# Kernel optimization log

Measured on AMD Instinct MI355X. Metric: run time of the kernel, lower is better.

Reference implementation:

```python
import jax, jax.numpy as jnp
import numpy as np

NUM_BINS = 8
TAIL = 3.0
MBW = 1e-3  # min_bin_width
MBH = 1e-3  # min_bin_height
MD = 1e-3   # min_derivative
B, C, H, W = 16, 12, 128, 128
COND = C // 3
HID = 64
STEP = 3 * NUM_BINS - 1
OUT = C * STEP


def setup_inputs() -> dict:
    key = jax.random.key(0)
    ks = jax.random.split(key, 8)
    s = lambda k, shape, scale=1.0: jax.random.normal(k, shape, jnp.float32) * scale
    return {
        'x': s(ks[0], (B, C, H, W)),
        'logdet': jnp.zeros((B,), jnp.float32),
        'conditioning': s(ks[1], (B, COND, H, W)),
        'W1': s(ks[2], (HID, C + COND, 3, 3), 0.05), 'b1': jnp.zeros((HID,), jnp.float32),
        'W2': s(ks[3], (HID, HID, 1, 1), 0.05), 'b2': jnp.zeros((HID,), jnp.float32),
        'W3': s(ks[4], (OUT, HID, 3, 3), 0.05), 'b3': jnp.zeros((OUT,), jnp.float32),
    }


def _conv(x, w, b, pad):
    y = jax.lax.conv_general_dilated(x, w, (1, 1), [(pad, pad), (pad, pad)],
                                     dimension_numbers=('NCHW', 'OIHW', 'NCHW'))
    return y + b[None, :, None, None]


def _checker_mask(h, w, parity):
    ii, jj = jnp.meshgrid(jnp.arange(h), jnp.arange(w), indexing='ij')
    m = jnp.where((ii + jj) % 2 == 0, parity, 1 - parity)
    return m.astype(jnp.float32)[None, None]  # (1,1,H,W)


def _rqs_forward(x, uw, uh, ud):
    # x: (B,C,H,W); uw/uh: (...,K); ud: (...,K-1). 'linear' tails, tail_bound=TAIL.
    K = NUM_BINS
    left, right = -TAIL, TAIL
    inside = (x >= left) & (x <= right)
    xc = jnp.clip(x, left, right)

    w = MBW + (1.0 - MBW * K) * jax.nn.softmax(uw, axis=-1)
    cw = jnp.pad(jnp.cumsum(w, -1), [(0, 0)] * (w.ndim - 1) + [(1, 0)])
    cw = (right - left) * cw + left
    cw = cw.at[..., 0].set(left).at[..., -1].set(right)
    w = cw[..., 1:] - cw[..., :-1]

    h = MBH + (1.0 - MBH * K) * jax.nn.softmax(uh, axis=-1)
    ch = jnp.pad(jnp.cumsum(h, -1), [(0, 0)] * (h.ndim - 1) + [(1, 0)])
    ch = (right - left) * ch + left
    ch = ch.at[..., 0].set(left).at[..., -1].set(right)
    h = ch[..., 1:] - ch[..., :-1]

    const = float(np.log(np.expm1(1.0 - MD)))  # boundary derivative -> 1 under linear tails
    udp = jnp.pad(ud, [(0, 0)] * (ud.ndim - 1) + [(1, 1)], constant_values=const)
    d = MD + jax.nn.softplus(udp)  # (...,K+1)

    delta = h / w
    # searchsorted: bin index per element
    idx = jnp.clip(jnp.sum((xc[..., None] >= cw).astype(jnp.int32), -1) - 1, 0, K - 1)[..., None]
    g = lambda t: jnp.take_along_axis(t, idx, axis=-1)[..., 0]

    icw, iw = g(cw), g(w)
    ich, ih = g(ch), g(h)
    idl = g(delta)
    id0 = g(d)
    id1 = g(d[..., 1:])

    theta = (xc - icw) / iw
    t1 = theta * (1.0 - theta)
    num = ih * (idl * theta ** 2 + id0 * t1)
    den = idl + (id0 + id1 - 2.0 * idl) * t1
    y = ich + num / den
    dnum = idl ** 2 * (id1 * theta ** 2 + 2.0 * idl * t1 + id0 * (1.0 - theta) ** 2)
    lad = jnp.log(dnum) - 2.0 * jnp.log(den)
    return jnp.where(inside, y, x), jnp.where(inside, lad, 0.0)


def reference(x, logdet, conditioning, W1, b1, W2, b2, W3, b3):
    mask = _checker_mask(H, W, 0)
    x_frozen = mask * x
    x_active = (1.0 - mask) * x
    z = jnp.concatenate([x_frozen, conditioning], axis=1)
    h1 = jax.nn.relu(_conv(z, W1, b1, 1))
    h2 = jax.nn.relu(_conv(h1, W2, b2, 0))
    params = _conv(h2, W3, b3, 1)  # (B, C*STEP, H, W)
    # all channels at once instead of python loop over C
    p = params.reshape(B, C, STEP, H, W).transpose(0, 1, 3, 4, 2)  # (B,C,H,W,STEP)
    uw = p[..., :NUM_BINS]
    uh = p[..., NUM_BINS:2 * NUM_BINS]
    ud = p[..., 2 * NUM_BINS:]
    y, lad = _rqs_forward(x_active, uw, uh, ud)
    x_out = x_frozen + y  # matches original: frozen part + spline output (no re-masking of y)
    logdet_out = logdet + lad.sum(axis=(1, 2, 3))
    return x_out, logdet_out
```

## Files before the change

kernel.cpp:

```cpp
#include <hip/hip_runtime.h>

#define HW (128*128)

typedef __bf16 bf16x8 __attribute__((ext_vector_type(8)));
typedef float  float4v __attribute__((ext_vector_type(4)));
typedef int    int4v   __attribute__((ext_vector_type(4)));
typedef int    int2v   __attribute__((ext_vector_type(2)));

static __device__ __forceinline__ short f2bf(float f) {
    unsigned u = __float_as_uint(f);
    unsigned r = (u + 0x7FFFu + ((u >> 16) & 1u)) >> 16;
    return (short)(r & 0xFFFFu);
}
static __device__ __forceinline__ int pack2(short a, short b) {
    return (int)((unsigned short)a | ((unsigned)(unsigned short)b << 16));
}
static __device__ __forceinline__ void async_cp16(const void* g, void* l) {
    __builtin_amdgcn_global_load_lds(
        (const __attribute__((address_space(1))) unsigned int*)g,
        (__attribute__((address_space(3))) unsigned int*)l, 16, 0, 0);
}

__global__ __launch_bounds__(256) void prep_weights(
    const float* __restrict__ W1, const float* __restrict__ W2,
    const float* __restrict__ W3,
    short* __restrict__ W1sw, short* __restrict__ W2sw, short* __restrict__ W3sw,
    char* __restrict__ h2p, int4v* __restrict__ zerobuf)
{
    int tid = blockIdx.x * 256 + threadIdx.x;
    int stride = gridDim.x * 256;
    for (int i = tid; i < 5*256*8; i += stride) {
        int e = i & 7, q = (i >> 3) & 255, s = i >> 11;
        int n = q >> 2, c = q & 3;
        int gc = c ^ ((n >> 1) & 3);
        int tap = 2*s + (gc >> 1);
        int ch = (gc & 1)*8 + e;
        float v = 0.f;
        if (tap < 9) {
            int ky = (tap*11) >> 5; int kx = tap - 3*ky;
            v = W1[((n*16 + ch)*3 + ky)*3 + kx];
        }
        W1sw[i] = f2bf(v);
    }
    for (int i = tid; i < 2*256*8; i += stride) {
        int e = i & 7, q = (i >> 3) & 255, s = i >> 11;
        int n = q >> 2, c = q & 3;
        int gc = c ^ ((n >> 1) & 3);
        int k = s*32 + gc*8 + e;
        W2sw[i] = f2bf(W2[n*64 + k]);
    }
    for (int i = tid; i < 9*288*64; i += stride) {
        int e = i & 7;
        int c = (i >> 3) & 7;
        int r = i >> 6;
        int tap = r / 288;
        int n = r - tap*288;
        int ch = n / 24, jj = n - 24*ch;
        int ci = ((c ^ (n & 7)) << 3) + e;
        float v = 0.f;
        if (jj < 23) v = W3[((ch*23 + jj)*64 + ci)*9 + tap];
        W3sw[i] = f2bf(v);
    }
    for (int i = tid; i < 64; i += stride) { int4v zz = {0,0,0,0}; zerobuf[i] = zz; }
    for (int i = tid; i < 16*516*8; i += stride) {
        int cchunk = i & 7, pxi = (i >> 3) % 516, b = i / (516*8);
        int yy, xx;
        if (pxi < 130)      { yy = 0;   xx = pxi; }
        else if (pxi < 260) { yy = 129; xx = pxi - 130; }
        else if (pxi < 388) { yy = pxi - 260 + 1; xx = 0; }
        else                { yy = pxi - 388 + 1; xx = 129; }
        int4v zz = {0,0,0,0};
        *(int4v*)(h2p + (size_t)((b*130 + yy)*130 + xx)*128 + cchunk*16) = zz;
    }
}

__global__ __launch_bounds__(256) void pack_z(
    const float* __restrict__ x, const float* __restrict__ cond,
    short* __restrict__ zp, float* __restrict__ ldslots)
{
    int id = blockIdx.x * 256 + threadIdx.x;
    if (id < 1024) ldslots[id] = 0.f;
    if (id >= 16*130*130) return;
    int b = id / 16900;
    int rem = id - b*16900;
    int yy = rem / 130;
    int xx = rem - yy*130;
    short vs[16];
    #pragma unroll
    for (int c = 0; c < 16; ++c) vs[c] = 0;
    if (yy >= 1 && yy <= 128 && xx >= 1 && xx <= 128) {
        int pix = (yy - 1)*128 + (xx - 1);
        bool frozen = ((yy + xx) & 1) == 1;
        #pragma unroll
        for (int c = 0; c < 12; ++c)
            vs[c] = f2bf(frozen ? x[(b*12 + c)*HW + pix] : 0.f);
        #pragma unroll
        for (int c = 0; c < 4; ++c)
            vs[12 + c] = f2bf(cond[(b*4 + c)*HW + pix]);
    }
    int4v lo = { pack2(vs[0],vs[1]),  pack2(vs[2],vs[3]),
                 pack2(vs[4],vs[5]),  pack2(vs[6],vs[7]) };
    int4v hi = { pack2(vs[8],vs[9]),  pack2(vs[10],vs[11]),
                 pack2(vs[12],vs[13]),pack2(vs[14],vs[15]) };
    *(int4v*)(zp + id*16)     = lo;
    *(int4v*)(zp + id*16 + 8) = hi;
}

__global__ __launch_bounds__(256, 4) void conv12_kernel(
    const char* __restrict__ zp, const char* __restrict__ W1sw,
    const char* __restrict__ W2sw,
    const float* __restrict__ b1, const float* __restrict__ b2,
    const char* __restrict__ zerobuf, char* __restrict__ h2p)
{
    __shared__ __align__(16) char smem[28672];
    int t = threadIdx.x;
    int lane = t & 63, w = t >> 6;
    int l15 = lane & 15, quad = lane >> 4;
    int bid = blockIdx.x;
    int b = bid & 15, y = bid >> 4;
    int chb = (w >> 1) * 32;
    int pxb = (w & 1) * 64;
    unsigned wbase = (unsigned)__builtin_amdgcn_readfirstlane(w << 10);

    int px1 = t >> 2;
    int gc1 = (t & 3) ^ ((px1 >> 1) & 3);
    int tl1 = gc1 >> 1, zoff1 = px1*32 + (gc1 & 1)*16;
    int q2 = t + 256;
    int px2 = q2 >> 2;
    int gc2 = (q2 & 3) ^ ((px2 >> 1) & 3);
    int tl2 = gc2 >> 1, zoff2 = px2*32 + (gc2 & 1)*16;

    int waddr[2], zaddr[4];
    #pragma unroll
    for (int i = 0; i < 2; ++i) {
        int n = chb + i*16 + l15;
        waddr[i] = 8192 + n*64 + ((quad ^ ((n >> 1) & 3)) << 4);
    }
    #pragma unroll
    for (int j = 0; j < 4; ++j) {
        int px = pxb + j*16 + l15;
        zaddr[j] = px*64 + ((quad ^ ((px >> 1) & 3)) << 4);
    }

    const char* zb = zp + (size_t)(b*16900)*32;
    const float4v z4 = {0.f,0.f,0.f,0.f};
    float4v acc[2][4];
    #pragma unroll
    for (int i = 0; i < 2; ++i)
        #pragma unroll
        for (int j = 0; j < 4; ++j) acc[i][j] = z4;

    for (int s = 0; s < 5; ++s) {
        __syncthreads();
        int ta = 2*s + tl1;
        const char* g1;
        if (ta < 9) { int ky = (ta*11) >> 5; int kx = ta - 3*ky;
            g1 = zb + ((y + ky)*130 + kx)*32 + zoff1; }
        else g1 = zerobuf + (lane << 4);
        async_cp16(g1, smem + wbase);
        int tb = 2*s + tl2;
        const char* g2;
        if (tb < 9) { int ky = (tb*11) >> 5; int kx = tb - 3*ky;
            g2 = zb + ((y + ky)*130 + kx)*32 + zoff2; }
        else g2 = zerobuf + (lane << 4);
        async_cp16(g2, smem + 4096 + wbase);
        async_cp16(W1sw + s*4096 + (t << 4), smem + 8192 + wbase);
        __syncthreads();
        bf16x8 aw[2];
        #pragma unroll
        for (int i = 0; i < 2; ++i) aw[i] = *(const bf16x8*)(smem + waddr[i]);
        #pragma unroll
        for (int j = 0; j < 4; ++j) {
            bf16x8 bzv = *(const bf16x8*)(smem + zaddr[j]);
            #pragma unroll
            for (int i = 0; i < 2; ++i)
                acc[i][j] = __builtin_amdgcn_mfma_f32_16x16x32_bf16(aw[i], bzv, acc[i][j], 0, 0, 0);
        }
    }
    {
        #pragma unroll
        for (int i = 0; i < 2; ++i) {
            int ch0 = chb + i*16 + quad*4;
            float bb0 = b1[ch0], bb1 = b1[ch0+1], bb2 = b1[ch0+2], bb3 = b1[ch0+3];
            #pragma unroll
            for (int j = 0; j < 4; ++j) {
                int px = pxb + j*16 + l15;
                short s0 = f2bf(fmaxf(acc[i][j][0] + bb0, 0.f));
                short s1 = f2bf(fmaxf(acc[i][j][1] + bb1, 0.f));
                short s2 = f2bf(fmaxf(acc[i][j][2] + bb2, 0.f));
                short s3 = f2bf(fmaxf(acc[i][j][3] + bb3, 0.f));
                int2v pk = { pack2(s0, s1), pack2(s2, s3) };
                *(int2v*)(smem + 12288 + px*128 + (((ch0 >> 3) ^ (px & 7)) << 4) + ((ch0 & 7) << 1)) = pk;
            }
        }
    }
    float4v acc2[2][4];
    #pragma unroll
    for (int i = 0; i < 2; ++i)
        #pragma unroll
        for (int j = 0; j < 4; ++j) acc2[i][j] = z4;
    for (int s = 0; s < 2; ++s) {
        __syncthreads();
        async_cp16(W2sw + s*4096 + (t << 4), smem + 8192 + wbase);
        __syncthreads();
        bf16x8 aw[2];
        #pragma unroll
        for (int i = 0; i < 2; ++i) aw[i] = *(const bf16x8*)(smem + waddr[i]);
        #pragma unroll
        for (int j = 0; j < 4; ++j) {
            int px = pxb + j*16 + l15;
            bf16x8 bh = *(const bf16x8*)(smem + 12288 + px*128 + (((s*4 + quad) ^ (px & 7)) << 4));
            #pragma unroll
            for (int i = 0; i < 2; ++i)
                acc2[i][j] = __builtin_amdgcn_mfma_f32_16x16x32_bf16(aw[i], bh, acc2[i][j], 0, 0, 0);
        }
    }
    __syncthreads();
    {
        #pragma unroll
        for (int i = 0; i < 2; ++i) {
            int ch0 = chb + i*16 + quad*4;
            float bb0 = b2[ch0], bb1 = b2[ch0+1], bb2 = b2[ch0+2], bb3 = b2[ch0+3];
            #pragma unroll
            for (int j = 0; j < 4; ++j) {
                int px = pxb + j*16 + l15;
                short s0 = f2bf(fmaxf(acc2[i][j][0] + bb0, 0.f));
                short s1 = f2bf(fmaxf(acc2[i][j][1] + bb1, 0.f));
                short s2 = f2bf(fmaxf(acc2[i][j][2] + bb2, 0.f));
                short s3 = f2bf(fmaxf(acc2[i][j][3] + bb3, 0.f));
                int2v pk = { pack2(s0, s1), pack2(s2, s3) };
                *(int2v*)(smem + 12288 + px*128 + (((ch0 >> 3) ^ (px & 7)) << 4) + ((ch0 & 7) << 1)) = pk;
            }
        }
    }
    __syncthreads();
    char* dst = h2p + ((size_t)(b*130 + y + 1)*130 + 1)*128;
    #pragma unroll
    for (int u = 0; u < 4; ++u) {
        int q = t + u*256;
        int px = q >> 3, g = q & 7;
        int4v v = *(const int4v*)(smem + 12288 + px*128 + ((g ^ (px & 7)) << 4));
        *(int4v*)(dst + px*128 + (g << 4)) = v;
    }
}

static __device__ __forceinline__ float rqs_eval(
    const float* __restrict__ pa, float xin, bool frozen, float& ldsum)
{
    float xa = frozen ? 0.f : xin;
    float xf = frozen ? xin : 0.f;
    float xc = fminf(fmaxf(xa, -3.f), 3.f);
    bool inside = (xa >= -3.f) && (xa <= 3.f);

    float mw = pa[0];
    #pragma unroll
    for (int j = 1; j < 8; ++j) mw = fmaxf(mw, pa[j]);
    float ew[8]; float sw = 0.f;
    #pragma unroll
    for (int j = 0; j < 8; ++j) { ew[j] = __expf(pa[j] - mw); sw += ew[j]; }
    float Aw = 0.992f / sw;
    float run = 0.f, cwl = -3.f, icw = -3.f, iwid = 1.f;
    int idx = 0;
    #pragma unroll
    for (int j = 0; j < 8; ++j) {
        float wj = fmaf(Aw, ew[j], 0.001f);
        run += wj;
        float cwr = (j == 7) ? 3.f : fmaf(6.f, run, -3.f);
        if (xc >= cwl) { icw = cwl; iwid = cwr - cwl; idx = j; }
        cwl = cwr;
    }
    float mh = pa[8];
    #pragma unroll
    for (int j = 9; j < 16; ++j) mh = fmaxf(mh, pa[j]);
    float eh[8]; float sh = 0.f;
    #pragma unroll
    for (int j = 0; j < 8; ++j) { eh[j] = __expf(pa[8 + j] - mh); sh += eh[j]; }
    float Ah = 0.992f / sh;
    run = 0.f;
    float chl = -3.f, ich = 0.f, ihei = 1.f;
    #pragma unroll
    for (int j = 0; j < 8; ++j) {
        float hj = fmaf(Ah, eh[j], 0.001f);
        run += hj;
        float chr = (j == 7) ? 3.f : fmaf(6.f, run, -3.f);
        if (j == idx) { ich = chl; ihei = chr - chl; }
        chl = chr;
    }
    float v0 = 0.f, v1 = 0.f;
    bool h0 = false, h1 = false;
    #pragma unroll
    for (int j = 1; j < 8; ++j) {
        float v = pa[15 + j];
        if (j == idx)     { v0 = v; h0 = true; }
        if (j == idx + 1) { v1 = v; h1 = true; }
    }
    float sp0 = (v0 > 15.f) ? v0 : __logf(1.f + __expf(v0));
    float sp1 = (v1 > 15.f) ? v1 : __logf(1.f + __expf(v1));
    float d0 = h0 ? (0.001f + sp0) : 1.f;
    float d1 = h1 ? (0.001f + sp1) : 1.f;

    float dl = ihei / iwid;
    float th = (xc - icw) / iwid;
    float omt = 1.f - th;
    float t1 = th * omt;
    float num = ihei * (dl*th*th + d0*t1);
    float den = dl + (d0 + d1 - 2.f*dl)*t1;
    float yv = ich + num/den;
    float dnum = dl*dl*(d1*th*th + 2.f*dl*t1 + d0*omt*omt);
    float lad = __logf(dnum) - 2.f*__logf(den);

    ldsum += inside ? lad : 0.f;
    return xf + (inside ? yv : xa);
}

__global__ __launch_bounds__(256, 6) void conv3_rqs_kernel(
    const char* __restrict__ h2p, const char* __restrict__ W3sw,
    const float* __restrict__ b3, const float* __restrict__ x,
    float* __restrict__ out, float* __restrict__ ldslots)
{
    __shared__ __align__(16) char smem[25600];
    int t = threadIdx.x;
    int lane = t & 63, w = t >> 6;
    int l15 = lane & 15, quad = lane >> 4;
    int bid = blockIdx.x;
    int b = bid & 15;
    int r0 = bid >> 4;
    int cg = r0 % 3;
    int r1 = r0 / 3;
    int ph = r1 & 1;
    int y = r1 >> 1;

    int u = w & 1, v = w >> 1;

    int aaddr[2], baddr[3];
    #pragma unroll
    for (int i = 0; i < 2; ++i) {
        int row = u*32 + i*16 + l15;
        aaddr[i] = row*128 + ((quad ^ (row & 7)) << 4);
    }
    #pragma unroll
    for (int j = 0; j < 3; ++j) {
        int nl = v*48 + j*16 + l15;
        baddr[j] = 8192 + nl*128 + ((quad ^ (nl & 7)) << 4);
    }

    int pxA0 = t >> 3, cA0 = t & 7;
    int offA0 = pxA0*128 + ((cA0 ^ (pxA0 & 7)) << 4);
    int q1 = t + 256;
    int pxA1 = q1 >> 3, cA1 = q1 & 7;
    int offA1 = pxA1*128 + ((cA1 ^ (pxA1 & 7)) << 4);
    unsigned wbase = (unsigned)__builtin_amdgcn_readfirstlane(w << 10);

    const float4v z4 = {0.f,0.f,0.f,0.f};
    float4v acc[2][3];
    #pragma unroll
    for (int i = 0; i < 2; ++i)
        #pragma unroll
        for (int j = 0; j < 3; ++j) acc[i][j] = z4;

    const char* h2pb = h2p + (size_t)(b*130)*130*128 + ph*8192;
    const char* W3b = W3sw + cg*12288;
    for (int tap = 0; tap < 9; ++tap) {
        int ty = (tap*11) >> 5;
        int tx = tap - 3*ty;
        const char* sbA = h2pb + ((y + ty)*130 + tx)*128;
        const char* sbB = W3b + tap*36864;
        __syncthreads();
        async_cp16(sbA + offA0, smem + wbase);
        async_cp16(sbA + offA1, smem + 4096 + wbase);
        async_cp16(sbB + (t << 4),        smem + 8192 + wbase);
        async_cp16(sbB + 4096 + (t << 4), smem + 12288 + wbase);
        async_cp16(sbB + 8192 + (t << 4), smem + 16384 + wbase);
        __syncthreads();
        #pragma unroll
        for (int kh = 0; kh < 2; ++kh) {
            int kx = kh << 6;
            bf16x8 av[2];
            #pragma unroll
            for (int i = 0; i < 2; ++i)
                av[i] = *(const bf16x8*)(smem + (aaddr[i] ^ kx));
            #pragma unroll
            for (int j = 0; j < 3; ++j) {
                bf16x8 bv = *(const bf16x8*)(smem + (baddr[j] ^ kx));
                #pragma unroll
                for (int i = 0; i < 2; ++i)
                    acc[i][j] = __builtin_amdgcn_mfma_f32_16x16x32_bf16(av[i], bv, acc[i][j], 0, 0, 0);
            }
        }
    }
    __syncthreads();

    float* scr = (float*)smem;
    #pragma unroll
    for (int i = 0; i < 2; ++i)
        #pragma unroll
        for (int j = 0; j < 3; ++j)
            #pragma unroll
            for (int r = 0; r < 4; ++r) {
                int row = u*32 + i*16 + quad*4 + r;
                int col = v*48 + j*16 + l15;
                scr[row*100 + col] = acc[i][j][r];
            }
    __syncthreads();

    int px = t & 63;
    int chl = w;
    int c = cg*4 + chl;
    const float* P = scr + px*100 + chl*24;
    float pa[23];
    {
        float pr[24];
        *(float4v*)&pr[0]  = *(const float4v*)(P);
        *(float4v*)&pr[4]  = *(const float4v*)(P + 4);
        *(float4v*)&pr[8]  = *(const float4v*)(P + 8);
        *(float4v*)&pr[12] = *(const float4v*)(P + 12);
        *(float4v*)&pr[16] = *(const float4v*)(P + 16);
        *(float4v*)&pr[20] = *(const float4v*)(P + 20);
        const float* bb3 = b3 + c*23;
        #pragma unroll
        for (int j = 0; j < 23; ++j) pa[j] = pr[j] + bb3[j];
    }
    int pxg = ph*64 + px;
    int gidx = ((b*12 + c) << 14) + (y << 7) + pxg;
    float xin = x[gidx];
    bool frozen = ((y + pxg) & 1) == 1;
    float ldsum = 0.f;
    out[gidx] = rqs_eval(pa, xin, frozen, ldsum);

    #pragma unroll
    for (int off = 32; off > 0; off >>= 1)
        ldsum += __shfl_down(ldsum, off, 64);
    if (lane == 0) atomicAdd(ldslots + b*64 + ((bid >> 4) & 63), ldsum);
}

__global__ __launch_bounds__(64) void logdet_reduce(
    const float* __restrict__ ldslots, const float* __restrict__ ld_in,
    float* __restrict__ ldout)
{
    int b = blockIdx.x;
    int lane = threadIdx.x;
    float s = ldslots[b*64 + lane];
    #pragma unroll
    for (int off = 32; off > 0; off >>= 1)
        s += __shfl_down(s, off, 64);
    if (lane == 0) ldout[b] = ld_in[b] + s;
}

extern "C" void kernel_launch(void* const* d_in, const int* in_sizes, int n_in,
                              void* d_out, int out_size, void* d_ws, size_t ws_size,
                              hipStream_t stream)
{
    (void)in_sizes; (void)n_in; (void)out_size; (void)ws_size;
    const float* x    = (const float*)d_in[0];
    const float* ld   = (const float*)d_in[1];
    const float* cond = (const float*)d_in[2];
    const float* W1   = (const float*)d_in[3];
    const float* b1   = (const float*)d_in[4];
    const float* W2   = (const float*)d_in[5];
    const float* b2   = (const float*)d_in[6];
    const float* W3   = (const float*)d_in[7];
    const float* b3   = (const float*)d_in[8];
    float* out = (float*)d_out;
    char* ws = (char*)d_ws;

    short* zp     = (short*)(ws);
    char*  h2p    = ws + 8652800;
    short* W1sw   = (short*)(ws + 43264000);
    short* W2sw   = (short*)(ws + 43284480);
    short* W3sw   = (short*)(ws + 43292672);
    char*  zerob  = ws + 43624448;
    float* ldslots= (float*)(ws + 43625472);
    float* ldout  = out + 12*HW*16;

    prep_weights<<<dim3(256), dim3(256), 0, stream>>>(
        W1, W2, W3, W1sw, W2sw, W3sw, h2p, (int4v*)zerob);
    pack_z<<<dim3(1057), dim3(256), 0, stream>>>(x, cond, zp, ldslots);
    conv12_kernel<<<dim3(2048), dim3(256), 0, stream>>>(
        (const char*)zp, (const char*)W1sw, (const char*)W2sw, b1, b2,
        (const char*)zerob, h2p);
    conv3_rqs_kernel<<<dim3(12288), dim3(256), 0, stream>>>(
        (const char*)h2p, (const char*)W3sw, b3, x, out, ldslots);
    logdet_reduce<<<dim3(16), dim3(64), 0, stream>>>(ldslots, ld, ldout);
}
```

Before: 216.5 us.

## Double conv3 pixel tile to a full 128-pixel row per block

Each conv3+RQS block now covers a whole 128-pixel image row instead of half a row. The weight tile loaded per tap is reused across twice as many pixels and the grid is halved, which cuts redundant weight traffic and per-block overhead. The cost is double the accumulator registers, so the occupancy hint drops from 6 to 4 blocks. The epilogue now stages the accumulators through shared memory in two rounds with extra barriers and a padded stride.

After: 209.9 us. 1.03x faster.

```diff
diff --git a/kernel.cpp b/kernel.cpp
--- a/kernel.cpp
+++ b/kernel.cpp
@@ -313,12 +313,12 @@
     return xf + (inside ? yv : xa);
 }
 
-__global__ __launch_bounds__(256, 6) void conv3_rqs_kernel(
+__global__ __launch_bounds__(256, 4) void conv3_rqs_kernel(
     const char* __restrict__ h2p, const char* __restrict__ W3sw,
     const float* __restrict__ b3, const float* __restrict__ x,
     float* __restrict__ out, float* __restrict__ ldslots)
 {
-    __shared__ __align__(16) char smem[25600];
+    __shared__ __align__(16) char smem[28672];
     int t = threadIdx.x;
     int lane = t & 63, w = t >> 6;
     int l15 = lane & 15, quad = lane >> 4;
@@ -326,39 +326,39 @@
     int b = bid & 15;
     int r0 = bid >> 4;
     int cg = r0 % 3;
-    int r1 = r0 / 3;
-    int ph = r1 & 1;
-    int y = r1 >> 1;
+    int y = r0 / 3;
 
     int u = w & 1, v = w >> 1;
 
-    int aaddr[2], baddr[3];
-    #pragma unroll
-    for (int i = 0; i < 2; ++i) {
-        int row = u*32 + i*16 + l15;
+    int aaddr[4], baddr[3];
+    #pragma unroll
+    for (int i = 0; i < 4; ++i) {
+        int row = u*64 + i*16 + l15;
         aaddr[i] = row*128 + ((quad ^ (row & 7)) << 4);
     }
     #pragma unroll
     for (int j = 0; j < 3; ++j) {
         int nl = v*48 + j*16 + l15;
-        baddr[j] = 8192 + nl*128 + ((quad ^ (nl & 7)) << 4);
-    }
-
-    int pxA0 = t >> 3, cA0 = t & 7;
-    int offA0 = pxA0*128 + ((cA0 ^ (pxA0 & 7)) << 4);
-    int q1 = t + 256;
-    int pxA1 = q1 >> 3, cA1 = q1 & 7;
-    int offA1 = pxA1*128 + ((cA1 ^ (pxA1 & 7)) << 4);
+        baddr[j] = 16384 + nl*128 + ((quad ^ (nl & 7)) << 4);
+    }
+
+    int offA[4];
+    #pragma unroll
+    for (int r = 0; r < 4; ++r) {
+        int q = t + r*256;
+        int px = q >> 3, c = q & 7;
+        offA[r] = px*128 + ((c ^ (px & 7)) << 4);
+    }
     unsigned wbase = (unsigned)__builtin_amdgcn_readfirstlane(w << 10);
 
     const float4v z4 = {0.f,0.f,0.f,0.f};
-    float4v acc[2][3];
-    #pragma unroll
-    for (int i = 0; i < 2; ++i)
+    float4v acc[4][3];
+    #pragma unroll
+    for (int i = 0; i < 4; ++i)
         #pragma unroll
         for (int j = 0; j < 3; ++j) acc[i][j] = z4;
 
-    const char* h2pb = h2p + (size_t)(b*130)*130*128 + ph*8192;
+    const char* h2pb = h2p + (size_t)(b*130)*130*128;
     const char* W3b = W3sw + cg*12288;
     for (int tap = 0; tap < 9; ++tap) {
         int ty = (tap*11) >> 5;
@@ -366,24 +366,25 @@
         const char* sbA = h2pb + ((y + ty)*130 + tx)*128;
         const char* sbB = W3b + tap*36864;
         __syncthreads();
-        async_cp16(sbA + offA0, smem + wbase);
-        async_cp16(sbA + offA1, smem + 4096 + wbase);
-        async_cp16(sbB + (t << 4),        smem + 8192 + wbase);
-        async_cp16(sbB + 4096 + (t << 4), smem + 12288 + wbase);
-        async_cp16(sbB + 8192 + (t << 4), smem + 16384 + wbase);
+        #pragma unroll
+        for (int r = 0; r < 4; ++r)
+            async_cp16(sbA + offA[r], smem + r*4096 + wbase);
+        #pragma unroll
+        for (int r = 0; r < 3; ++r)
+            async_cp16(sbB + r*4096 + (t << 4), smem + 16384 + r*4096 + wbase);
         __syncthreads();
         #pragma unroll
         for (int kh = 0; kh < 2; ++kh) {
             int kx = kh << 6;
-            bf16x8 av[2];
-            #pragma unroll
-            for (int i = 0; i < 2; ++i)
+            bf16x8 av[4];
+            #pragma unroll
+            for (int i = 0; i < 4; ++i)
                 av[i] = *(const bf16x8*)(smem + (aaddr[i] ^ kx));
             #pragma unroll
             for (int j = 0; j < 3; ++j) {
                 bf16x8 bv = *(const bf16x8*)(smem + (baddr[j] ^ kx));
                 #pragma unroll
-                for (int i = 0; i < 2; ++i)
+                for (int i = 0; i < 4; ++i)
                     acc[i][j] = __builtin_amdgcn_mfma_f32_16x16x32_bf16(av[i], bv, acc[i][j], 0, 0, 0);
             }
         }
@@ -391,46 +392,51 @@
     __syncthreads();
 
     float* scr = (float*)smem;
-    #pragma unroll
-    for (int i = 0; i < 2; ++i)
-        #pragma unroll
-        for (int j = 0; j < 3; ++j)
-            #pragma unroll
-            for (int r = 0; r < 4; ++r) {
-                int row = u*32 + i*16 + quad*4 + r;
-                int col = v*48 + j*16 + l15;
-                scr[row*100 + col] = acc[i][j][r];
-            }
-    __syncthreads();
-
-    int px = t & 63;
-    int chl = w;
+    float ldsum = 0.f;
+    int pxl = t & 63;
+    int chl = t >> 6;
     int c = cg*4 + chl;
-    const float* P = scr + px*100 + chl*24;
-    float pa[23];
-    {
-        float pr[24];
-        *(float4v*)&pr[0]  = *(const float4v*)(P);
-        *(float4v*)&pr[4]  = *(const float4v*)(P + 4);
-        *(float4v*)&pr[8]  = *(const float4v*)(P + 8);
-        *(float4v*)&pr[12] = *(const float4v*)(P + 12);
-        *(float4v*)&pr[16] = *(const float4v*)(P + 16);
-        *(float4v*)&pr[20] = *(const float4v*)(P + 20);
-        const float* bb3 = b3 + c*23;
-        #pragma unroll
-        for (int j = 0; j < 23; ++j) pa[j] = pr[j] + bb3[j];
-    }
-    int pxg = ph*64 + px;
-    int gidx = ((b*12 + c) << 14) + (y << 7) + pxg;
-    float xin = x[gidx];
-    bool frozen = ((y + pxg) & 1) == 1;
-    float ldsum = 0.f;
-    out[gidx] = rqs_eval(pa, xin, frozen, ldsum);
-
+    const float* bb3 = b3 + c*23;
+
+    #pragma unroll
+    for (int rnd = 0; rnd < 2; ++rnd) {
+        if (u == rnd) {
+            #pragma unroll
+            for (int i = 0; i < 4; ++i)
+                #pragma unroll
+                for (int j = 0; j < 3; ++j)
+                    #pragma unroll
+                    for (int r = 0; r < 4; ++r) {
+                        int row = i*16 + quad*4 + r;
+                        int col = v*48 + j*16 + l15;
+                        scr[row*104 + col] = acc[i][j][r];
+                    }
+        }
+        __syncthreads();
+        const float* P = scr + pxl*104 + chl*24;
+        float pa[23];
+        {
+            float pr[24];
+            *(float4v*)&pr[0]  = *(const float4v*)(P);
+            *(float4v*)&pr[4]  = *(const float4v*)(P + 4);
+            *(float4v*)&pr[8]  = *(const float4v*)(P + 8);
+            *(float4v*)&pr[12] = *(const float4v*)(P + 12);
+            *(float4v*)&pr[16] = *(const float4v*)(P + 16);
+            *(float4v*)&pr[20] = *(const float4v*)(P + 20);
+            #pragma unroll
+            for (int j = 0; j < 23; ++j) pa[j] = pr[j] + bb3[j];
+        }
+        int pxg = rnd*64 + pxl;
+        int gidx = ((b*12 + c) << 14) + (y << 7) + pxg;
+        float xin = x[gidx];
+        bool frozen = ((y + pxg) & 1) == 1;
+        out[gidx] = rqs_eval(pa, xin, frozen, ldsum);
+        __syncthreads();
+    }
     #pragma unroll
     for (int off = 32; off > 0; off >>= 1)
         ldsum += __shfl_down(ldsum, off, 64);
-    if (lane == 0) atomicAdd(ldslots + b*64 + ((bid >> 4) & 63), ldsum);
+    if (lane == 0) atomicAdd(ldslots + b*64 + (r0 & 63), ldsum);
 }
 
 __global__ __launch_bounds__(64) void logdet_reduce(
@@ -478,7 +484,7 @@
     conv12_kernel<<<dim3(2048), dim3(256), 0, stream>>>(
         (const char*)zp, (const char*)W1sw, (const char*)W2sw, b1, b2,
         (const char*)zerob, h2p);
-    conv3_rqs_kernel<<<dim3(12288), dim3(256), 0, stream>>>(
+    conv3_rqs_kernel<<<dim3(6144), dim3(256), 0, stream>>>(
         (const char*)h2p, (const char*)W3sw, b3, x, out, ldslots);
     logdet_reduce<<<dim3(16), dim3(64), 0, stream>>>(ldslots, ld, ldout);
 }
```
